# Optimization experiments

Hardware: AMD Instinct MI355X
Metric: run time of the kernel (lower is better)

Reference implementation:

```python
import jax, jax.numpy as jnp
import numpy as np

T = 35            # cfg.VOXEL_POINT_COUNT
D, H, W = 10, 400, 352  # cfg.INPUT_DEPTH/HEIGHT/WIDTH
EPS = 1e-5


def _vfe(x, mask, w, b, gamma, beta):
    # x: [K, T, Cin]; mask: [K, T, 1]
    h = jax.nn.relu(jnp.einsum('ktc,cu->ktu', x, w) + b)        # [K, T, U]
    mean = jnp.mean(h, axis=(0, 1))
    var = jnp.var(h, axis=(0, 1))
    h = (h - mean) * jax.lax.rsqrt(var + EPS) * gamma + beta    # batch-stat BN
    agg = jnp.max(h, axis=1, keepdims=True)                     # [K, 1, U]
    cat = jnp.concatenate([h, jnp.broadcast_to(agg, h.shape)], axis=-1)  # [K, T, 2U]
    return cat * mask


def setup_inputs() -> dict:
    key = jax.random.key(0)
    ks = jax.random.split(key, 12)
    K = 40000
    feature = jax.random.normal(ks[0], (K, T, 7), dtype=jnp.float32)
    # zero out ~half the points so the nonzero mask is meaningful
    keep = jax.random.bernoulli(ks[1], 0.5, (K, T, 1)).astype(jnp.float32)
    feature = feature * keep
    bidx = jax.random.randint(ks[2], (K, 1), 0, 2)
    didx = jax.random.randint(ks[3], (K, 1), 0, D)
    hidx = jax.random.randint(ks[4], (K, 1), 0, H)
    widx = jax.random.randint(ks[5], (K, 1), 0, W)
    coordinate = jnp.concatenate([bidx, didx, hidx, widx], axis=1).astype(jnp.int32)
    s = 0.1
    return {
        'feature': feature,
        'w1': jax.random.normal(ks[6], (7, 16), dtype=jnp.float32) * s,
        'b1': jnp.zeros((16,), dtype=jnp.float32),
        'gamma1': jnp.ones((16,), dtype=jnp.float32),
        'beta1': jnp.zeros((16,), dtype=jnp.float32),
        'w2': jax.random.normal(ks[7], (32, 32), dtype=jnp.float32) * s,
        'b2': jnp.zeros((32,), dtype=jnp.float32),
        'gamma2': jnp.ones((32,), dtype=jnp.float32),
        'beta2': jnp.zeros((32,), dtype=jnp.float32),
        'coordinate': coordinate,
        'batch_size': 2,
    }


def reference(feature, w1, b1, gamma1, beta1, w2, b2, gamma2, beta2, coordinate, batch_size):
    # mask: voxel point is valid if any channel nonzero (max over channels != 0)
    mask = (jnp.max(feature, axis=2, keepdims=True) != 0).astype(feature.dtype)  # [K, T, 1]
    x = _vfe(feature, mask, w1, b1, gamma1, beta1)   # [K, T, 32]
    x = _vfe(x, mask, w2, b2, gamma2, beta2)         # [K, T, 64]
    voxelwise = jnp.max(x, axis=1)                   # [K, 64]
    out = jnp.zeros((batch_size, D, H, W, 64), dtype=voxelwise.dtype)
    out = out.at[coordinate[:, 0], coordinate[:, 1], coordinate[:, 2], coordinate[:, 3]].add(voxelwise)
    return out
```

## Files before the change

kernel.cpp:

```cpp
#include <hip/hip_runtime.h>
#include <math.h>

#define TT 35
#define DD 10
#define HD 400
#define WD 352
#define CIN 7
#define U1 16
#define U2 32
#define EPSV 1e-5f

#define WS_SUM1 256
#define WS_SSQ1 768
#define WS_SUM2 1280
#define WS_SSQ2 1792
#define NC1 32
#define NC2 16
#define WS_ZERO_FLOATS 2304
#define WS_SUM_OFF 4096

typedef __bf16 bf16x8 __attribute__((ext_vector_type(8)));
typedef float f32x4 __attribute__((ext_vector_type(4)));

__device__ inline unsigned short f2bf(float x) {
  unsigned u = __builtin_bit_cast(unsigned, x);
  unsigned r = (u + 0x7fff + ((u >> 16) & 1)) >> 16;
  return (unsigned short)r;
}

__global__ __launch_bounds__(256) void k_stats1(
    const float* __restrict__ feat, const float* __restrict__ w1,
    const float* __restrict__ b1, float* __restrict__ ws, int P) {
  __shared__ float s_w1[CIN * U1];
  __shared__ float s_b1[U1];
  __shared__ float s_red[4][2 * U1];

  int tid = threadIdx.x;
  if (tid < CIN * U1) s_w1[tid] = w1[tid];
  if (tid < U1) s_b1[tid] = b1[tid];
  __syncthreads();

  float sum[U1], ssq[U1];
#pragma unroll
  for (int u = 0; u < U1; ++u) { sum[u] = 0.f; ssq[u] = 0.f; }

  int stride = gridDim.x * blockDim.x;
  for (int p = blockIdx.x * blockDim.x + tid; p < P; p += stride) {
    const float* f = feat + (size_t)p * CIN;
    float x[CIN];
#pragma unroll
    for (int c = 0; c < CIN; ++c) x[c] = f[c];
#pragma unroll
    for (int u = 0; u < U1; ++u) {
      float acc = s_b1[u];
#pragma unroll
      for (int c = 0; c < CIN; ++c) acc += x[c] * s_w1[c * U1 + u];
      float h = fmaxf(acc, 0.f);
      sum[u] += h;
      ssq[u] += h * h;
    }
  }

  int lane = tid & 63, wv = tid >> 6;
#pragma unroll
  for (int u = 0; u < U1; ++u) {
    float s = sum[u], q = ssq[u];
    for (int off = 32; off; off >>= 1) {
      s += __shfl_down(s, off);
      q += __shfl_down(q, off);
    }
    if (lane == 0) { s_red[wv][u] = s; s_red[wv][U1 + u] = q; }
  }
  __syncthreads();
  if (tid < 2 * U1) {
    float tot = s_red[0][tid] + s_red[1][tid] + s_red[2][tid] + s_red[3][tid];
    int copy = blockIdx.x & (NC1 - 1);
    int u = tid & (U1 - 1);
    int base = (tid < U1) ? WS_SUM1 : WS_SSQ1;
    atomicAdd(&ws[base + copy * U1 + u], tot);
  }
}

__global__ __launch_bounds__(256) void k_vfe2(
    const float* __restrict__ feat, const float* __restrict__ w1,
    const float* __restrict__ b1, const float* __restrict__ g1,
    const float* __restrict__ be1, const float* __restrict__ w2,
    const float* __restrict__ b2, float* __restrict__ ws,
    float* __restrict__ sumg, float* __restrict__ cntg, int K, float invN,
    int G) {
  __shared__ unsigned short s_w2b[32 * 40];
  __shared__ unsigned short s_catb[4][48][32];
  __shared__ float s_mk[4][40];
  __shared__ float s_red[4][64];
  __shared__ float s_A1[U1], s_B1[U1];

  int tid = threadIdx.x;
  int lane = tid & 63, wv = tid >> 6;
  int g = lane >> 4, u = lane & 15;

  for (int i = tid; i < 32 * 32; i += 256) {
    int n = i >> 5, cp = i & 31;
    int c = (cp & 1) ? (16 + (cp >> 1)) : (cp >> 1);
    s_w2b[n * 40 + cp] = f2bf(w2[c * 32 + n]);
  }
  {
    unsigned* z = (unsigned*)s_catb;
    for (int i = tid; i < 4 * 13 * 16; i += 256) {
      int w = i / 208, rem = i % 208;
      int row = 35 + (rem >> 4), k = rem & 15;
      z[(w * 48 + row) * 16 + k] = 0u;
    }
  }
  if (tid < 32) {
    int ch = tid & 15;
    int base = (tid < 16) ? WS_SUM1 : WS_SSQ1;
    float acc = 0.f;
#pragma unroll
    for (int c = 0; c < NC1; ++c) acc += ws[base + c * U1 + ch];
    s_red[0][tid] = acc;
  }
  __syncthreads();
  if (tid < 16) {
    float s = s_red[0][tid], q = s_red[0][16 + tid];
    float mean = s * invN;
    float var = q * invN - mean * mean;
    float A = g1[tid] / sqrtf(var + EPSV);
    s_A1[tid] = A;
    s_B1[tid] = be1[tid] - mean * A;
  }
  __syncthreads();

  float A1 = s_A1[u], B1 = s_B1[u];
  float w1r[CIN];
#pragma unroll
  for (int c = 0; c < CIN; ++c) w1r[c] = w1[c * U1 + u];
  float b1u = b1[u];
  float b2c[2] = {b2[u], b2[16 + u]};
  bf16x8 bfr[2];
#pragma unroll
  for (int nt = 0; nt < 2; ++nt) {
    uint4 raw = *(const uint4*)&s_w2b[(nt * 16 + u) * 40 + g * 8];
    bfr[nt] = __builtin_bit_cast(bf16x8, raw);
  }

  for (int grp = blockIdx.x; grp < G; grp += gridDim.x) {
    __syncthreads();
    int v = grp * 4 + wv;
    bool active = (v < K);

    float h1n[9], mkv[9];
    float aggl = -INFINITY;
    float cntl = 0.f;
    const float* fv = feat + (size_t)v * (TT * CIN);
#pragma unroll
    for (int j = 0; j < 9; ++j) {
      int t = g + 4 * j;
      h1n[j] = -INFINITY;
      mkv[j] = 0.f;
      if (active && t < TT) {
        const float* fr = fv + t * CIN;
        float x0 = fr[0], x1 = fr[1], x2 = fr[2], x3 = fr[3];
        float x4 = fr[4], x5 = fr[5], x6 = fr[6];
        float m = fmaxf(fmaxf(fmaxf(x0, x1), fmaxf(x2, x3)),
                        fmaxf(fmaxf(x4, x5), x6));
        float mk = (m != 0.f) ? 1.f : 0.f;
        float acc = b1u + x0 * w1r[0] + x1 * w1r[1] + x2 * w1r[2] +
                    x3 * w1r[3] + x4 * w1r[4] + x5 * w1r[5] + x6 * w1r[6];
        float h = fmaxf(acc, 0.f);
        h1n[j] = A1 * h + B1;
        mkv[j] = mk;
        cntl += mk;
        if (u == 0) s_mk[wv][t] = mk;
        aggl = fmaxf(aggl, h1n[j]);
      }
    }
    aggl = fmaxf(aggl, __shfl_xor(aggl, 16));
    aggl = fmaxf(aggl, __shfl_xor(aggl, 32));
    cntl += __shfl_xor(cntl, 16);
    cntl += __shfl_xor(cntl, 32);
    if (active && lane == 0) cntg[v] = cntl;

#pragma unroll
    for (int j = 0; j < 9; ++j) {
      int t = g + 4 * j;
      if (active && t < TT) {
        unsigned pk = (unsigned)f2bf(h1n[j] * mkv[j]) |
                      ((unsigned)f2bf(aggl * mkv[j]) << 16);
        *(unsigned*)&s_catb[wv][t][2 * u] = pk;
      }
    }

    f32x4 acc[2][3];
#pragma unroll
    for (int nt = 0; nt < 2; ++nt)
#pragma unroll
      for (int mt = 0; mt < 3; ++mt) acc[nt][mt] = (f32x4)(0.f);
#pragma unroll
    for (int mt = 0; mt < 3; ++mt) {
      uint4 raw = *(const uint4*)&s_catb[wv][mt * 16 + u][g * 8];
      bf16x8 afr = __builtin_bit_cast(bf16x8, raw);
#pragma unroll
      for (int nt = 0; nt < 2; ++nt)
        acc[nt][mt] = __builtin_amdgcn_mfma_f32_16x16x32_bf16(afr, bfr[nt],
                                                              acc[nt][mt], 0, 0, 0);
    }

    float sum[2] = {0.f, 0.f}, ssq[2] = {0.f, 0.f};
    float maxm[2] = {-INFINITY, -INFINITY}, minm[2] = {INFINITY, INFINITY};
    float maxa[2] = {-INFINITY, -INFINITY}, mina[2] = {INFINITY, INFINITY};
#pragma unroll
    for (int nt = 0; nt < 2; ++nt) {
#pragma unroll
      for (int mt = 0; mt < 3; ++mt) {
#pragma unroll
        for (int r = 0; r < 4; ++r) {
          int row = mt * 16 + g * 4 + r;
          if (row < TT) {
            float h = fmaxf(acc[nt][mt][r] + b2c[nt], 0.f);
            sum[nt] += h;
            ssq[nt] += h * h;
            maxa[nt] = fmaxf(maxa[nt], h);
            mina[nt] = fminf(mina[nt], h);
            float mk = s_mk[wv][row];
            if (mk != 0.f) {
              maxm[nt] = fmaxf(maxm[nt], h);
              minm[nt] = fminf(minm[nt], h);
            }
          }
        }
      }
    }

#pragma unroll
    for (int nt = 0; nt < 2; ++nt) {
      sum[nt] += __shfl_xor(sum[nt], 16);
      sum[nt] += __shfl_xor(sum[nt], 32);
      ssq[nt] += __shfl_xor(ssq[nt], 16);
      ssq[nt] += __shfl_xor(ssq[nt], 32);
      maxa[nt] = fmaxf(maxa[nt], __shfl_xor(maxa[nt], 16));
      maxa[nt] = fmaxf(maxa[nt], __shfl_xor(maxa[nt], 32));
      mina[nt] = fminf(mina[nt], __shfl_xor(mina[nt], 16));
      mina[nt] = fminf(mina[nt], __shfl_xor(mina[nt], 32));
      maxm[nt] = fmaxf(maxm[nt], __shfl_xor(maxm[nt], 16));
      maxm[nt] = fmaxf(maxm[nt], __shfl_xor(maxm[nt], 32));
      minm[nt] = fminf(minm[nt], __shfl_xor(minm[nt], 16));
      minm[nt] = fminf(minm[nt], __shfl_xor(minm[nt], 32));
    }
    if (active && g == 0) {
#pragma unroll
      for (int nt = 0; nt < 2; ++nt) {
        float4 sm = make_float4(maxm[nt], minm[nt], maxa[nt], mina[nt]);
        *(float4*)&sumg[(size_t)v * 128 + (nt * 16 + u) * 4] = sm;
      }
    }

    float contrib = 0.f;
    if (active) {
      contrib = (g == 0) ? sum[0] : (g == 1) ? sum[1] : (g == 2) ? ssq[0] : ssq[1];
    }
    s_red[wv][(g & 1) * 16 + u + (g >> 1) * 32] = contrib;
    __syncthreads();
    if (tid < 64) {
      float tot = s_red[0][tid] + s_red[1][tid] + s_red[2][tid] + s_red[3][tid];
      int copy = blockIdx.x & (NC2 - 1);
      int ch = tid & 31;
      int base = (tid < 32) ? WS_SUM2 : WS_SSQ2;
      atomicAdd(&ws[base + copy * U2 + ch], tot);
    }
  }
}

__global__ __launch_bounds__(256) void k_final(
    const float* __restrict__ sumg, const float* __restrict__ cntg,
    const float* __restrict__ ws, const float* __restrict__ g2,
    const float* __restrict__ be2, const int* __restrict__ coord,
    float* __restrict__ out, int K, float invN) {
  __shared__ float s_tmp[64];
  __shared__ float s_A2[U2], s_B2[U2];
  int tid = threadIdx.x;

  if (tid < 64) {
    int ch = tid & 31;
    int base = (tid < 32) ? WS_SUM2 : WS_SSQ2;
    float acc = 0.f;
#pragma unroll
    for (int c = 0; c < NC2; ++c) acc += ws[base + c * U2 + ch];
    s_tmp[tid] = acc;
  }
  __syncthreads();
  if (tid < 32) {
    float mean = s_tmp[tid] * invN;
    float var = s_tmp[32 + tid] * invN - mean * mean;
    float A = g2[tid] / sqrtf(var + EPSV);
    s_A2[tid] = A;
    s_B2[tid] = be2[tid] - mean * A;
  }
  __syncthreads();

  int v = blockIdx.x * 8 + (tid >> 5);
  int ch = tid & 31;
  if (v < K) {
    float A2 = s_A2[ch], B2 = s_B2[ch];
    float4 sm = *(const float4*)&sumg[(size_t)v * 128 + ch * 4];
    float cnt = cntg[v];

    float hm = (A2 >= 0.f) ? (A2 * sm.x + B2) : (A2 * sm.y + B2);
    float ag = (A2 >= 0.f) ? (A2 * sm.z + B2) : (A2 * sm.w + B2);
    float voxr = (cnt < 0.5f) ? 0.f : ((cnt > TT - 0.5f) ? hm : fmaxf(hm, 0.f));
    float voxa = (cnt < 0.5f) ? 0.f : ((cnt > TT - 0.5f) ? ag : fmaxf(ag, 0.f));

    const int4 cd = *(const int4*)&coord[4 * v];
    long base = ((((long)cd.x * DD + cd.y) * HD + cd.z) * WD + cd.w) * 64;
    atomicAdd(&out[base + ch], voxr);
    atomicAdd(&out[base + 32 + ch], voxa);
  }
}

extern "C" void kernel_launch(void* const* d_in, const int* in_sizes, int n_in,
                              void* d_out, int out_size, void* d_ws,
                              size_t ws_size, hipStream_t stream) {
  const float* feat = (const float*)d_in[0];
  const float* w1 = (const float*)d_in[1];
  const float* b1 = (const float*)d_in[2];
  const float* g1 = (const float*)d_in[3];
  const float* be1 = (const float*)d_in[4];
  const float* w2 = (const float*)d_in[5];
  const float* b2 = (const float*)d_in[6];
  const float* g2 = (const float*)d_in[7];
  const float* be2 = (const float*)d_in[8];
  const int* coord = (const int*)d_in[9];
  float* out = (float*)d_out;
  float* ws = (float*)d_ws;

  int K = in_sizes[0] / (TT * CIN);
  int P = K * TT;
  float invN = 1.0f / (float)P;

  float* sumg = ws + WS_SUM_OFF;
  float* cntg = sumg + (size_t)K * 128;

  (void)hipMemsetAsync(d_out, 0, (size_t)out_size * sizeof(float), stream);
  (void)hipMemsetAsync(d_ws, 0, WS_ZERO_FLOATS * sizeof(float), stream);

  k_stats1<<<2048, 256, 0, stream>>>(feat, w1, b1, ws, P);

  int G = (K + 3) / 4;
  int vb = (G + 3) / 4;
  k_vfe2<<<vb, 256, 0, stream>>>(feat, w1, b1, g1, be1, w2, b2, ws, sumg, cntg,
                                 K, invN, G);
  k_final<<<(K + 7) / 8, 256, 0, stream>>>(sumg, cntg, ws, g2, be2, coord, out,
                                           K, invN);
}
```

Before: 842.2 us.

## Fuse three kernels into one persistent kernel with grid barriers and in-kernel output zeroing

Merges the stats, VFE2 and scatter kernels into a single persistent kernel of 768 blocks separated by software grid barriers. The output memset is dropped; instead one wave per block zeroes the output while the other three waves run the VFE2 voxel work. Per-block shared-memory reductions and syncthreads are replaced with direct per-wave atomics spread over more copies. This removes launch gaps and the separate memset, but relies on all 768 blocks being co-resident and gives up one wave of compute during phase two.

```diff
diff --git a/kernel.cpp b/kernel.cpp
--- a/kernel.cpp
+++ b/kernel.cpp
@@ -9,15 +9,17 @@
 #define U1 16
 #define U2 32
 #define EPSV 1e-5f
+#define NB 768
 
 #define WS_SUM1 256
 #define WS_SSQ1 768
 #define WS_SUM2 1280
-#define WS_SSQ2 1792
+#define WS_SSQ2 3328
 #define NC1 32
-#define NC2 16
-#define WS_ZERO_FLOATS 2304
-#define WS_SUM_OFF 4096
+#define NC2 64
+#define WS_BAR 5376
+#define WS_ZERO_FLOATS 5392
+#define WS_SUM_OFF 8192
 
 typedef __bf16 bf16x8 __attribute__((ext_vector_type(8)));
 typedef float f32x4 __attribute__((ext_vector_type(4)));
@@ -28,75 +30,55 @@
   return (unsigned short)r;
 }
 
-__global__ __launch_bounds__(256) void k_stats1(
-    const float* __restrict__ feat, const float* __restrict__ w1,
-    const float* __restrict__ b1, float* __restrict__ ws, int P) {
-  __shared__ float s_w1[CIN * U1];
-  __shared__ float s_b1[U1];
-  __shared__ float s_red[4][2 * U1];
-
-  int tid = threadIdx.x;
-  if (tid < CIN * U1) s_w1[tid] = w1[tid];
-  if (tid < U1) s_b1[tid] = b1[tid];
-  __syncthreads();
-
-  float sum[U1], ssq[U1];
-#pragma unroll
-  for (int u = 0; u < U1; ++u) { sum[u] = 0.f; ssq[u] = 0.f; }
-
-  int stride = gridDim.x * blockDim.x;
-  for (int p = blockIdx.x * blockDim.x + tid; p < P; p += stride) {
-    const float* f = feat + (size_t)p * CIN;
-    float x[CIN];
-#pragma unroll
-    for (int c = 0; c < CIN; ++c) x[c] = f[c];
-#pragma unroll
-    for (int u = 0; u < U1; ++u) {
-      float acc = s_b1[u];
-#pragma unroll
-      for (int c = 0; c < CIN; ++c) acc += x[c] * s_w1[c * U1 + u];
-      float h = fmaxf(acc, 0.f);
-      sum[u] += h;
-      ssq[u] += h * h;
-    }
-  }
-
-  int lane = tid & 63, wv = tid >> 6;
-#pragma unroll
-  for (int u = 0; u < U1; ++u) {
-    float s = sum[u], q = ssq[u];
-    for (int off = 32; off; off >>= 1) {
-      s += __shfl_down(s, off);
-      q += __shfl_down(q, off);
-    }
-    if (lane == 0) { s_red[wv][u] = s; s_red[wv][U1 + u] = q; }
-  }
-  __syncthreads();
-  if (tid < 2 * U1) {
-    float tot = s_red[0][tid] + s_red[1][tid] + s_red[2][tid] + s_red[3][tid];
-    int copy = blockIdx.x & (NC1 - 1);
-    int u = tid & (U1 - 1);
-    int base = (tid < U1) ? WS_SUM1 : WS_SSQ1;
-    atomicAdd(&ws[base + copy * U1 + u], tot);
-  }
-}
-
-__global__ __launch_bounds__(256) void k_vfe2(
+__device__ inline float aload(const float* p) {
+  return __hip_atomic_load(p, __ATOMIC_RELAXED, __HIP_MEMORY_SCOPE_AGENT);
+}
+
+__device__ inline void grid_barrier(int* cnt, int* gen, int nb) {
+  __threadfence();
+  __syncthreads();
+  if (threadIdx.x == 0) {
+    int g0 = __hip_atomic_load(gen, __ATOMIC_RELAXED, __HIP_MEMORY_SCOPE_AGENT);
+    int t = __hip_atomic_fetch_add(cnt, 1, __ATOMIC_ACQ_REL,
+                                   __HIP_MEMORY_SCOPE_AGENT);
+    if (t == nb - 1) {
+      __hip_atomic_store(cnt, 0, __ATOMIC_RELAXED, __HIP_MEMORY_SCOPE_AGENT);
+      __hip_atomic_fetch_add(gen, 1, __ATOMIC_RELEASE,
+                             __HIP_MEMORY_SCOPE_AGENT);
+    } else {
+      while (__hip_atomic_load(gen, __ATOMIC_ACQUIRE,
+                               __HIP_MEMORY_SCOPE_AGENT) == g0) {
+        __builtin_amdgcn_s_sleep(16);
+      }
+    }
+  }
+  __syncthreads();
+  __threadfence();
+}
+
+__global__ __launch_bounds__(256, 4) void k_fused(
     const float* __restrict__ feat, const float* __restrict__ w1,
     const float* __restrict__ b1, const float* __restrict__ g1,
     const float* __restrict__ be1, const float* __restrict__ w2,
-    const float* __restrict__ b2, float* __restrict__ ws,
-    float* __restrict__ sumg, float* __restrict__ cntg, int K, float invN,
-    int G) {
+    const float* __restrict__ b2, const float* __restrict__ g2,
+    const float* __restrict__ be2, const int* __restrict__ coord,
+    float* __restrict__ ws, float* __restrict__ sumg,
+    float* __restrict__ cntg, float* __restrict__ out, long n4, int K,
+    float invN, int P) {
   __shared__ unsigned short s_w2b[32 * 40];
-  __shared__ unsigned short s_catb[4][48][32];
-  __shared__ float s_mk[4][40];
-  __shared__ float s_red[4][64];
+  __shared__ unsigned short s_catb[3][48][32];
+  __shared__ float s_mk[3][40];
+  __shared__ float s_redA[4][32];
+  __shared__ float s_fin[64];
   __shared__ float s_A1[U1], s_B1[U1];
+  __shared__ float s_A2[U2], s_B2[U2];
+  __shared__ float s_w1f[CIN * U1 + U1];
 
   int tid = threadIdx.x;
   int lane = tid & 63, wv = tid >> 6;
   int g = lane >> 4, u = lane & 15;
+  int nb = gridDim.x;
+  int* bar = (int*)(ws + WS_BAR);
 
   for (int i = tid; i < 32 * 32; i += 256) {
     int n = i >> 5, cp = i & 31;
@@ -105,23 +87,69 @@
   }
   {
     unsigned* z = (unsigned*)s_catb;
-    for (int i = tid; i < 4 * 13 * 16; i += 256) {
+    for (int i = tid; i < 3 * 13 * 16; i += 256) {
       int w = i / 208, rem = i % 208;
       int row = 35 + (rem >> 4), k = rem & 15;
       z[(w * 48 + row) * 16 + k] = 0u;
     }
   }
+  if (tid < CIN * U1) s_w1f[tid] = w1[tid];
+  if (tid < U1) s_w1f[CIN * U1 + tid] = b1[tid];
+  __syncthreads();
+
+  {
+    float sum[U1], ssq[U1];
+#pragma unroll
+    for (int c = 0; c < U1; ++c) { sum[c] = 0.f; ssq[c] = 0.f; }
+    int stride = nb * 256;
+    for (int p = blockIdx.x * 256 + tid; p < P; p += stride) {
+      const float* f = feat + (size_t)p * CIN;
+      float x[CIN];
+#pragma unroll
+      for (int c = 0; c < CIN; ++c) x[c] = f[c];
+#pragma unroll
+      for (int uu = 0; uu < U1; ++uu) {
+        float acc = s_w1f[CIN * U1 + uu];
+#pragma unroll
+        for (int c = 0; c < CIN; ++c) acc += x[c] * s_w1f[c * U1 + uu];
+        float h = fmaxf(acc, 0.f);
+        sum[uu] += h;
+        ssq[uu] += h * h;
+      }
+    }
+#pragma unroll
+    for (int uu = 0; uu < U1; ++uu) {
+      float s = sum[uu], q = ssq[uu];
+      for (int off = 32; off; off >>= 1) {
+        s += __shfl_down(s, off);
+        q += __shfl_down(q, off);
+      }
+      if (lane == 0) { s_redA[wv][uu] = s; s_redA[wv][U1 + uu] = q; }
+    }
+    __syncthreads();
+    if (tid < 2 * U1) {
+      float tot =
+          s_redA[0][tid] + s_redA[1][tid] + s_redA[2][tid] + s_redA[3][tid];
+      int copy = blockIdx.x & (NC1 - 1);
+      int uu = tid & (U1 - 1);
+      int base = (tid < U1) ? WS_SUM1 : WS_SSQ1;
+      atomicAdd(&ws[base + copy * U1 + uu], tot);
+    }
+  }
+
+  grid_barrier(&bar[0], &bar[1], nb);
+
   if (tid < 32) {
     int ch = tid & 15;
     int base = (tid < 16) ? WS_SUM1 : WS_SSQ1;
     float acc = 0.f;
 #pragma unroll
-    for (int c = 0; c < NC1; ++c) acc += ws[base + c * U1 + ch];
-    s_red[0][tid] = acc;
+    for (int c = 0; c < NC1; ++c) acc += aload(&ws[base + c * U1 + ch]);
+    s_fin[tid] = acc;
   }
   __syncthreads();
   if (tid < 16) {
-    float s = s_red[0][tid], q = s_red[0][16 + tid];
+    float s = s_fin[tid], q = s_fin[16 + tid];
     float mean = s * invN;
     float var = q * invN - mean * mean;
     float A = g1[tid] / sqrtf(var + EPSV);
@@ -130,189 +158,185 @@
   }
   __syncthreads();
 
-  float A1 = s_A1[u], B1 = s_B1[u];
-  float w1r[CIN];
-#pragma unroll
-  for (int c = 0; c < CIN; ++c) w1r[c] = w1[c * U1 + u];
-  float b1u = b1[u];
-  float b2c[2] = {b2[u], b2[16 + u]};
-  bf16x8 bfr[2];
-#pragma unroll
-  for (int nt = 0; nt < 2; ++nt) {
-    uint4 raw = *(const uint4*)&s_w2b[(nt * 16 + u) * 40 + g * 8];
-    bfr[nt] = __builtin_bit_cast(bf16x8, raw);
-  }
-
-  for (int grp = blockIdx.x; grp < G; grp += gridDim.x) {
-    __syncthreads();
-    int v = grp * 4 + wv;
-    bool active = (v < K);
-
-    float h1n[9], mkv[9];
-    float aggl = -INFINITY;
-    float cntl = 0.f;
-    const float* fv = feat + (size_t)v * (TT * CIN);
-#pragma unroll
-    for (int j = 0; j < 9; ++j) {
-      int t = g + 4 * j;
-      h1n[j] = -INFINITY;
-      mkv[j] = 0.f;
-      if (active && t < TT) {
-        const float* fr = fv + t * CIN;
-        float x0 = fr[0], x1 = fr[1], x2 = fr[2], x3 = fr[3];
-        float x4 = fr[4], x5 = fr[5], x6 = fr[6];
-        float m = fmaxf(fmaxf(fmaxf(x0, x1), fmaxf(x2, x3)),
-                        fmaxf(fmaxf(x4, x5), x6));
-        float mk = (m != 0.f) ? 1.f : 0.f;
-        float acc = b1u + x0 * w1r[0] + x1 * w1r[1] + x2 * w1r[2] +
-                    x3 * w1r[3] + x4 * w1r[4] + x5 * w1r[5] + x6 * w1r[6];
-        float h = fmaxf(acc, 0.f);
-        h1n[j] = A1 * h + B1;
-        mkv[j] = mk;
-        cntl += mk;
-        if (u == 0) s_mk[wv][t] = mk;
-        aggl = fmaxf(aggl, h1n[j]);
-      }
-    }
-    aggl = fmaxf(aggl, __shfl_xor(aggl, 16));
-    aggl = fmaxf(aggl, __shfl_xor(aggl, 32));
-    cntl += __shfl_xor(cntl, 16);
-    cntl += __shfl_xor(cntl, 32);
-    if (active && lane == 0) cntg[v] = cntl;
-
-#pragma unroll
-    for (int j = 0; j < 9; ++j) {
-      int t = g + 4 * j;
-      if (active && t < TT) {
-        unsigned pk = (unsigned)f2bf(h1n[j] * mkv[j]) |
-                      ((unsigned)f2bf(aggl * mkv[j]) << 16);
-        *(unsigned*)&s_catb[wv][t][2 * u] = pk;
-      }
-    }
-
-    f32x4 acc[2][3];
-#pragma unroll
-    for (int nt = 0; nt < 2; ++nt)
-#pragma unroll
-      for (int mt = 0; mt < 3; ++mt) acc[nt][mt] = (f32x4)(0.f);
-#pragma unroll
-    for (int mt = 0; mt < 3; ++mt) {
-      uint4 raw = *(const uint4*)&s_catb[wv][mt * 16 + u][g * 8];
-      bf16x8 afr = __builtin_bit_cast(bf16x8, raw);
+  if (wv == 3) {
+    float4* out4 = (float4*)out;
+    float4 zz = make_float4(0.f, 0.f, 0.f, 0.f);
+    long stride = (long)nb * 64;
+    for (long i = (long)blockIdx.x * 64 + lane; i < n4; i += stride) out4[i] = zz;
+  } else {
+    float A1 = s_A1[u], B1 = s_B1[u];
+    float w1r[CIN];
+#pragma unroll
+    for (int c = 0; c < CIN; ++c) w1r[c] = w1[c * U1 + u];
+    float b1u = b1[u];
+    float b2c[2] = {b2[u], b2[16 + u]};
+    bf16x8 bfr[2];
+#pragma unroll
+    for (int nt = 0; nt < 2; ++nt) {
+      uint4 raw = *(const uint4*)&s_w2b[(nt * 16 + u) * 40 + g * 8];
+      bfr[nt] = __builtin_bit_cast(bf16x8, raw);
+    }
+    int copy = (blockIdx.x * 3 + wv) & (NC2 - 1);
+
+    for (int vbase = blockIdx.x * 3; vbase < K; vbase += nb * 3) {
+      int v = vbase + wv;
+      bool active = (v < K);
+
+      float h1n[9], mkv[9];
+      float aggl = -INFINITY;
+      float cntl = 0.f;
+      const float* fv = feat + (size_t)v * (TT * CIN);
+#pragma unroll
+      for (int j = 0; j < 9; ++j) {
+        int t = g + 4 * j;
+        h1n[j] = -INFINITY;
+        mkv[j] = 0.f;
+        if (active && t < TT) {
+          const float* fr = fv + t * CIN;
+          float x0 = fr[0], x1 = fr[1], x2 = fr[2], x3 = fr[3];
+          float x4 = fr[4], x5 = fr[5], x6 = fr[6];
+          float m = fmaxf(fmaxf(fmaxf(x0, x1), fmaxf(x2, x3)),
+                          fmaxf(fmaxf(x4, x5), x6));
+          float mk = (m != 0.f) ? 1.f : 0.f;
+          float acc = b1u + x0 * w1r[0] + x1 * w1r[1] + x2 * w1r[2] +
+                      x3 * w1r[3] + x4 * w1r[4] + x5 * w1r[5] + x6 * w1r[6];
+          float h = fmaxf(acc, 0.f);
+          h1n[j] = A1 * h + B1;
+          mkv[j] = mk;
+          cntl += mk;
+          if (u == 0) s_mk[wv][t] = mk;
+          aggl = fmaxf(aggl, h1n[j]);
+        }
+      }
+      aggl = fmaxf(aggl, __shfl_xor(aggl, 16));
+      aggl = fmaxf(aggl, __shfl_xor(aggl, 32));
+      cntl += __shfl_xor(cntl, 16);
+      cntl += __shfl_xor(cntl, 32);
+      if (active && lane == 0) cntg[v] = cntl;
+
+#pragma unroll
+      for (int j = 0; j < 9; ++j) {
+        int t = g + 4 * j;
+        if (active && t < TT) {
+          unsigned pk = (unsigned)f2bf(h1n[j] * mkv[j]) |
+                        ((unsigned)f2bf(aggl * mkv[j]) << 16);
+          *(unsigned*)&s_catb[wv][t][2 * u] = pk;
+        }
+      }
+
+      f32x4 acc[2][3];
 #pragma unroll
       for (int nt = 0; nt < 2; ++nt)
-        acc[nt][mt] = __builtin_amdgcn_mfma_f32_16x16x32_bf16(afr, bfr[nt],
-                                                              acc[nt][mt], 0, 0, 0);
-    }
-
-    float sum[2] = {0.f, 0.f}, ssq[2] = {0.f, 0.f};
-    float maxm[2] = {-INFINITY, -INFINITY}, minm[2] = {INFINITY, INFINITY};
-    float maxa[2] = {-INFINITY, -INFINITY}, mina[2] = {INFINITY, INFINITY};
-#pragma unroll
-    for (int nt = 0; nt < 2; ++nt) {
+#pragma unroll
+        for (int mt = 0; mt < 3; ++mt) acc[nt][mt] = (f32x4)(0.f);
 #pragma unroll
       for (int mt = 0; mt < 3; ++mt) {
-#pragma unroll
-        for (int r = 0; r < 4; ++r) {
-          int row = mt * 16 + g * 4 + r;
-          if (row < TT) {
-            float h = fmaxf(acc[nt][mt][r] + b2c[nt], 0.f);
-            sum[nt] += h;
-            ssq[nt] += h * h;
-            maxa[nt] = fmaxf(maxa[nt], h);
-            mina[nt] = fminf(mina[nt], h);
-            float mk = s_mk[wv][row];
-            if (mk != 0.f) {
-              maxm[nt] = fmaxf(maxm[nt], h);
-              minm[nt] = fminf(minm[nt], h);
+        uint4 raw = *(const uint4*)&s_catb[wv][mt * 16 + u][g * 8];
+        bf16x8 afr = __builtin_bit_cast(bf16x8, raw);
+#pragma unroll
+        for (int nt = 0; nt < 2; ++nt)
+          acc[nt][mt] = __builtin_amdgcn_mfma_f32_16x16x32_bf16(
+              afr, bfr[nt], acc[nt][mt], 0, 0, 0);
+      }
+
+      float sum[2] = {0.f, 0.f}, ssq[2] = {0.f, 0.f};
+      float maxm[2] = {-INFINITY, -INFINITY}, minm[2] = {INFINITY, INFINITY};
+      float maxa[2] = {-INFINITY, -INFINITY}, mina[2] = {INFINITY, INFINITY};
+#pragma unroll
+      for (int nt = 0; nt < 2; ++nt) {
+#pragma unroll
+        for (int mt = 0; mt < 3; ++mt) {
+#pragma unroll
+          for (int r = 0; r < 4; ++r) {
+            int row = mt * 16 + g * 4 + r;
+            if (row < TT) {
+              float h = fmaxf(acc[nt][mt][r] + b2c[nt], 0.f);
+              sum[nt] += h;
+              ssq[nt] += h * h;
+              maxa[nt] = fmaxf(maxa[nt], h);
+              mina[nt] = fminf(mina[nt], h);
+              float mk = s_mk[wv][row];
+              if (mk != 0.f) {
+                maxm[nt] = fmaxf(maxm[nt], h);
+                minm[nt] = fminf(minm[nt], h);
+              }
             }
           }
         }
       }
-    }
-
-#pragma unroll
-    for (int nt = 0; nt < 2; ++nt) {
-      sum[nt] += __shfl_xor(sum[nt], 16);
-      sum[nt] += __shfl_xor(sum[nt], 32);
-      ssq[nt] += __shfl_xor(ssq[nt], 16);
-      ssq[nt] += __shfl_xor(ssq[nt], 32);
-      maxa[nt] = fmaxf(maxa[nt], __shfl_xor(maxa[nt], 16));
-      maxa[nt] = fmaxf(maxa[nt], __shfl_xor(maxa[nt], 32));
-      mina[nt] = fminf(mina[nt], __shfl_xor(mina[nt], 16));
-      mina[nt] = fminf(mina[nt], __shfl_xor(mina[nt], 32));
-      maxm[nt] = fmaxf(maxm[nt], __shfl_xor(maxm[nt], 16));
-      maxm[nt] = fmaxf(maxm[nt], __shfl_xor(maxm[nt], 32));
-      minm[nt] = fminf(minm[nt], __shfl_xor(minm[nt], 16));
-      minm[nt] = fminf(minm[nt], __shfl_xor(minm[nt], 32));
-    }
-    if (active && g == 0) {
 #pragma unroll
       for (int nt = 0; nt < 2; ++nt) {
-        float4 sm = make_float4(maxm[nt], minm[nt], maxa[nt], mina[nt]);
-        *(float4*)&sumg[(size_t)v * 128 + (nt * 16 + u) * 4] = sm;
-      }
-    }
-
-    float contrib = 0.f;
-    if (active) {
-      contrib = (g == 0) ? sum[0] : (g == 1) ? sum[1] : (g == 2) ? ssq[0] : ssq[1];
-    }
-    s_red[wv][(g & 1) * 16 + u + (g >> 1) * 32] = contrib;
-    __syncthreads();
-    if (tid < 64) {
-      float tot = s_red[0][tid] + s_red[1][tid] + s_red[2][tid] + s_red[3][tid];
-      int copy = blockIdx.x & (NC2 - 1);
-      int ch = tid & 31;
-      int base = (tid < 32) ? WS_SUM2 : WS_SSQ2;
-      atomicAdd(&ws[base + copy * U2 + ch], tot);
-    }
-  }
-}
-
-__global__ __launch_bounds__(256) void k_final(
-    const float* __restrict__ sumg, const float* __restrict__ cntg,
-    const float* __restrict__ ws, const float* __restrict__ g2,
-    const float* __restrict__ be2, const int* __restrict__ coord,
-    float* __restrict__ out, int K, float invN) {
-  __shared__ float s_tmp[64];
-  __shared__ float s_A2[U2], s_B2[U2];
-  int tid = threadIdx.x;
+        sum[nt] += __shfl_xor(sum[nt], 16);
+        sum[nt] += __shfl_xor(sum[nt], 32);
+        ssq[nt] += __shfl_xor(ssq[nt], 16);
+        ssq[nt] += __shfl_xor(ssq[nt], 32);
+        maxa[nt] = fmaxf(maxa[nt], __shfl_xor(maxa[nt], 16));
+        maxa[nt] = fmaxf(maxa[nt], __shfl_xor(maxa[nt], 32));
+        mina[nt] = fminf(mina[nt], __shfl_xor(mina[nt], 16));
+        mina[nt] = fminf(mina[nt], __shfl_xor(mina[nt], 32));
+        maxm[nt] = fmaxf(maxm[nt], __shfl_xor(maxm[nt], 16));
+        maxm[nt] = fmaxf(maxm[nt], __shfl_xor(maxm[nt], 32));
+        minm[nt] = fminf(minm[nt], __shfl_xor(minm[nt], 16));
+        minm[nt] = fminf(minm[nt], __shfl_xor(minm[nt], 32));
+      }
+      if (active) {
+        if (g == 0) {
+#pragma unroll
+          for (int nt = 0; nt < 2; ++nt) {
+            float4 sm = make_float4(maxm[nt], minm[nt], maxa[nt], mina[nt]);
+            *(float4*)&sumg[(size_t)v * 128 + (nt * 16 + u) * 4] = sm;
+          }
+        }
+        float contrib = (g == 0) ? sum[0]
+                      : (g == 1) ? sum[1]
+                      : (g == 2) ? ssq[0] : ssq[1];
+        int ch = ((g & 1) << 4) + u;
+        int base = (g < 2) ? WS_SUM2 : WS_SSQ2;
+        atomicAdd(&ws[base + copy * U2 + ch], contrib);
+      }
+    }
+  }
+
+  grid_barrier(&bar[2], &bar[3], nb);
 
   if (tid < 64) {
     int ch = tid & 31;
     int base = (tid < 32) ? WS_SUM2 : WS_SSQ2;
     float acc = 0.f;
 #pragma unroll
-    for (int c = 0; c < NC2; ++c) acc += ws[base + c * U2 + ch];
-    s_tmp[tid] = acc;
+    for (int c = 0; c < NC2; ++c) acc += aload(&ws[base + c * U2 + ch]);
+    s_fin[tid] = acc;
   }
   __syncthreads();
   if (tid < 32) {
-    float mean = s_tmp[tid] * invN;
-    float var = s_tmp[32 + tid] * invN - mean * mean;
+    float mean = s_fin[tid] * invN;
+    float var = s_fin[32 + tid] * invN - mean * mean;
     float A = g2[tid] / sqrtf(var + EPSV);
     s_A2[tid] = A;
     s_B2[tid] = be2[tid] - mean * A;
   }
   __syncthreads();
 
-  int v = blockIdx.x * 8 + (tid >> 5);
-  int ch = tid & 31;
-  if (v < K) {
+  {
+    int ch = tid & 31;
     float A2 = s_A2[ch], B2 = s_B2[ch];
-    float4 sm = *(const float4*)&sumg[(size_t)v * 128 + ch * 4];
-    float cnt = cntg[v];
-
-    float hm = (A2 >= 0.f) ? (A2 * sm.x + B2) : (A2 * sm.y + B2);
-    float ag = (A2 >= 0.f) ? (A2 * sm.z + B2) : (A2 * sm.w + B2);
-    float voxr = (cnt < 0.5f) ? 0.f : ((cnt > TT - 0.5f) ? hm : fmaxf(hm, 0.f));
-    float voxa = (cnt < 0.5f) ? 0.f : ((cnt > TT - 0.5f) ? ag : fmaxf(ag, 0.f));
-
-    const int4 cd = *(const int4*)&coord[4 * v];
-    long base = ((((long)cd.x * DD + cd.y) * HD + cd.z) * WD + cd.w) * 64;
-    atomicAdd(&out[base + ch], voxr);
-    atomicAdd(&out[base + 32 + ch], voxa);
+    for (int v0 = blockIdx.x * 8; v0 < K; v0 += nb * 8) {
+      int v = v0 + (tid >> 5);
+      if (v < K) {
+        float4 sm = *(const float4*)&sumg[(size_t)v * 128 + ch * 4];
+        float cnt = cntg[v];
+        float hm = (A2 >= 0.f) ? (A2 * sm.x + B2) : (A2 * sm.y + B2);
+        float ag = (A2 >= 0.f) ? (A2 * sm.z + B2) : (A2 * sm.w + B2);
+        float voxr =
+            (cnt < 0.5f) ? 0.f : ((cnt > TT - 0.5f) ? hm : fmaxf(hm, 0.f));
+        float voxa =
+            (cnt < 0.5f) ? 0.f : ((cnt > TT - 0.5f) ? ag : fmaxf(ag, 0.f));
+        const int4 cd = *(const int4*)&coord[4 * v];
+        long base = ((((long)cd.x * DD + cd.y) * HD + cd.z) * WD + cd.w) * 64;
+        atomicAdd(&out[base + ch], voxr);
+        atomicAdd(&out[base + 32 + ch], voxa);
+      }
+    }
   }
 }
 
@@ -335,19 +359,13 @@
   int K = in_sizes[0] / (TT * CIN);
   int P = K * TT;
   float invN = 1.0f / (float)P;
+  long n4 = (long)out_size / 4;
 
   float* sumg = ws + WS_SUM_OFF;
   float* cntg = sumg + (size_t)K * 128;
 
-  (void)hipMemsetAsync(d_out, 0, (size_t)out_size * sizeof(float), stream);
   (void)hipMemsetAsync(d_ws, 0, WS_ZERO_FLOATS * sizeof(float), stream);
 
-  k_stats1<<<2048, 256, 0, stream>>>(feat, w1, b1, ws, P);
-
-  int G = (K + 3) / 4;
-  int vb = (G + 3) / 4;
-  k_vfe2<<<vb, 256, 0, stream>>>(feat, w1, b1, g1, be1, w2, b2, ws, sumg, cntg,
-                                 K, invN, G);
-  k_final<<<(K + 7) / 8, 256, 0, stream>>>(sumg, cntg, ws, g2, be2, coord, out,
-                                           K, invN);
-}
+  k_fused<<<NB, 256, 0, stream>>>(feat, w1, b1, g1, be1, w2, b2, g2, be2,
+                                  coord, ws, sumg, cntg, out, n4, K, invN, P);
+}
```

Measured after the change: 1.409 ms. 1.67x slower.
